# Performance work log

Measured on AMD Instinct MI355X. Metric: run time of the kernel, lower is better.

The kernel has to match this reference:

```python
import jax, jax.numpy as jnp
import numpy as np

T, B, D_IN, H = 512, 2048, 128, 16  # seq_len, batch, input_dim, hidden_dim == n_qubits


def _gate(z, theta):
    # Analytic result of the variational circuit:
    # RX(z_i) then RX(theta_i) on |0>, CNOT ladder, PauliZ on every wire
    # => <Z_k> = prod_{j<=k} cos(z_j + theta_j)
    return jnp.cumprod(jnp.cos(z + theta), axis=-1)


def setup_inputs() -> dict:
    key = jax.random.key(0)
    ks = jax.random.split(key, 13)
    fan_in = D_IN + H
    s = 1.0 / np.sqrt(fan_in)
    inputs = jax.random.normal(ks[0], (T, B, D_IN), dtype=jnp.float32)
    def lin(k):
        k1, k2 = jax.random.split(k)
        W = jax.random.uniform(k1, (H, fan_in), jnp.float32, -s, s)
        b = jax.random.uniform(k2, (H,), jnp.float32, -s, s)
        return W, b
    Wf, bf = lin(ks[1]); Wi, bi = lin(ks[2]); Wu, bu = lin(ks[3]); Wo, bo = lin(ks[4])
    theta_f = jax.random.uniform(ks[5], (H,), jnp.float32, 0.0, 2 * np.pi)
    theta_i = jax.random.uniform(ks[6], (H,), jnp.float32, 0.0, 2 * np.pi)
    theta_u = jax.random.uniform(ks[7], (H,), jnp.float32, 0.0, 2 * np.pi)
    theta_o = jax.random.uniform(ks[8], (H,), jnp.float32, 0.0, 2 * np.pi)
    return {"inputs": inputs,
            "Wf": Wf, "bf": bf, "Wi": Wi, "bi": bi,
            "Wu": Wu, "bu": bu, "Wo": Wo, "bo": bo,
            "theta_f": theta_f, "theta_i": theta_i,
            "theta_u": theta_u, "theta_o": theta_o}


def reference(inputs, Wf, bf, Wi, bi, Wu, bu, Wo, bo,
              theta_f, theta_i, theta_u, theta_o):
    Bsz = inputs.shape[1]
    h0 = jnp.zeros((Bsz, H), inputs.dtype)
    c0 = jnp.zeros((Bsz, H), inputs.dtype)

    def step(carry, x_t):
        hx, cx = carry
        comb = jnp.concatenate([x_t, hx], axis=1)          # (B, D_IN+H)
        f = jax.nn.sigmoid(_gate(comb @ Wf.T + bf, theta_f))
        i = jax.nn.sigmoid(_gate(comb @ Wi.T + bi, theta_i))
        g = jnp.tanh(_gate(comb @ Wu.T + bu, theta_u))
        o = jax.nn.sigmoid(_gate(comb @ Wo.T + bo, theta_o))
        cx = f * cx + i * g
        hx = o * jnp.tanh(cx)
        return (hx, cx), hx

    (hx, cx), outputs = jax.lax.scan(step, (h0, c0), inputs)
    return outputs, hx, cx
```

## Files before the change

kernel.cpp:

```cpp
#include <hip/hip_runtime.h>

#define T_STEPS 512
#define BATCH   2048
#define DIN     128
#define NH      16
#define COMB    (DIN + NH)

__device__ __forceinline__ float rcpf(float x)  { return __builtin_amdgcn_rcpf(x); }
__device__ __forceinline__ float sigmf(float x) { return rcpf(1.f + __expf(-x)); }
__device__ __forceinline__ float tanhf_(float x){ float e = __expf(2.f * x); return (e - 1.f) * rcpf(e + 1.f); }

template <int D>
__device__ __forceinline__ float scan_shr(float v) {
    int r = __builtin_amdgcn_update_dpp(0x3f800000, __float_as_int(v),
                                        0x110 | D, 0xF, 0xF, false);
    return __int_as_float(r);
}

__global__ __launch_bounds__(64, 2) void qlstm_kernel(
    const float* __restrict__ x,
    const float* __restrict__ Wf, const float* __restrict__ bf,
    const float* __restrict__ Wi, const float* __restrict__ bi,
    const float* __restrict__ Wu, const float* __restrict__ bu,
    const float* __restrict__ Wo, const float* __restrict__ bo,
    const float* __restrict__ thf, const float* __restrict__ thi,
    const float* __restrict__ thu, const float* __restrict__ tho,
    float* __restrict__ out)
{
    const int lane = threadIdx.x;
    const int k    = lane & 15;
    const int q    = lane >> 4;
    const int b    = blockIdx.x;

    const float* Wg[4] = {Wf, Wi, Wu, Wo};
    const float* bg[4] = {bf, bi, bu, bo};
    const float* tg[4] = {thf, thi, thu, tho};

    float w[4][32], wh[4][4], bt[4];
#pragma unroll
    for (int g = 0; g < 4; ++g) {
        const float* Wr = Wg[g] + k * COMB;
#pragma unroll
        for (int j = 0; j < 32; ++j) w[g][j] = Wr[q * 32 + j];
#pragma unroll
        for (int kk = 0; kk < 4; ++kk) wh[g][kk] = Wr[DIN + q * 4 + kk];
        bt[g] = bg[g][k] + tg[g][k];
    }

    float h = 0.f, c = 0.f;
    float cvA[32], cvB[32];

    auto xrow = [&](int t) -> const float* {
        return x + ((size_t)t * BATCH + b) * DIN + q * 32;
    };
    auto loadx = [&](float (&cv)[32], const float* p) {
#pragma unroll
        for (int j4 = 0; j4 < 8; ++j4) {
            const float4 v = *(const float4*)(p + j4 * 4);
            cv[j4 * 4 + 0] = v.x; cv[j4 * 4 + 1] = v.y;
            cv[j4 * 4 + 2] = v.z; cv[j4 * 4 + 3] = v.w;
        }
    };

    float* op = out + (size_t)b * NH + k;

    auto step = [&](int t, float (&cv)[32]) {
        float acc[4] = {0.f, 0.f, 0.f, 0.f};
#pragma unroll
        for (int j = 0; j < 32; ++j) {
#pragma unroll
            for (int g = 0; g < 4; ++g) acc[g] += cv[j] * w[g][j];
        }
#pragma unroll
        for (int kk = 0; kk < 4; ++kk) {
            const float hv = __shfl(h, q * 4 + kk, 64);
#pragma unroll
            for (int g = 0; g < 4; ++g) acc[g] += hv * wh[g][kk];
        }
#pragma unroll
        for (int g = 0; g < 4; ++g) {
            acc[g] += __shfl_xor(acc[g], 16, 64);
            acc[g] += __shfl_xor(acc[g], 32, 64);
            acc[g] = __cosf(acc[g] + bt[g]);
        }
#pragma unroll
        for (int g = 0; g < 4; ++g) {
            acc[g] *= scan_shr<1>(acc[g]);
            acc[g] *= scan_shr<2>(acc[g]);
            acc[g] *= scan_shr<4>(acc[g]);
            acc[g] *= scan_shr<8>(acc[g]);
        }
        const float f  = sigmf(acc[0]);
        const float i_ = sigmf(acc[1]);
        const float u  = tanhf_(acc[2]);
        const float o  = sigmf(acc[3]);
        c = f * c + i_ * u;
        h = o * tanhf_(c);
        if (q == 0) *op = h;
        op += (size_t)BATCH * NH;
    };

    loadx(cvA, xrow(0));
    for (int t = 0; t < T_STEPS; t += 2) {
        loadx(cvB, xrow(t + 1));
        step(t, cvA);
        const int tn = (t + 2 < T_STEPS) ? t + 2 : T_STEPS - 1;
        loadx(cvA, xrow(tn));
        step(t + 1, cvB);
    }

    if (q == 0) {
        const size_t base = (size_t)T_STEPS * BATCH * NH;
        out[base + (size_t)b * NH + k] = h;
        out[base + (size_t)BATCH * NH + (size_t)b * NH + k] = c;
    }
}

extern "C" void kernel_launch(void* const* d_in, const int* in_sizes, int n_in,
                              void* d_out, int out_size, void* d_ws, size_t ws_size,
                              hipStream_t stream) {
    const float* x   = (const float*)d_in[0];
    const float* Wf  = (const float*)d_in[1];
    const float* bf  = (const float*)d_in[2];
    const float* Wi  = (const float*)d_in[3];
    const float* bi  = (const float*)d_in[4];
    const float* Wu  = (const float*)d_in[5];
    const float* bu  = (const float*)d_in[6];
    const float* Wo  = (const float*)d_in[7];
    const float* bo  = (const float*)d_in[8];
    const float* thf = (const float*)d_in[9];
    const float* thi = (const float*)d_in[10];
    const float* thu = (const float*)d_in[11];
    const float* tho = (const float*)d_in[12];

    qlstm_kernel<<<dim3(BATCH), dim3(64), 0, stream>>>(
        x, Wf, bf, Wi, bi, Wu, bu, Wo, bo, thf, thi, thu, tho, (float*)d_out);
}
```

Measured before the change: 1.166 ms.

## Split input projection into a parallel pre-pass and lean recurrent kernel

Adds a zx_kernel that computes the input-to-gate projections (x·W plus bias and theta) for a chunk of timesteps in parallel and writes them to workspace. The recurrent kernel then handles only the 16-wide hidden matmul per step, with one lane per gate×unit, readlane broadcasts of h, a unified sigmoid/tanh activation, and bpermute gathers. This takes the large input matmul off the serial critical path. In exchange it writes and re-reads an extra 256 MB intermediate through HBM and depends on workspace size, falling back to the old kernel when no workspace is available.

```diff
diff --git a/kernel.cpp b/kernel.cpp
--- a/kernel.cpp
+++ b/kernel.cpp
@@ -5,6 +5,7 @@
 #define DIN     128
 #define NH      16
 #define COMB    (DIN + NH)
+#define G64     64
 
 __device__ __forceinline__ float rcpf(float x)  { return __builtin_amdgcn_rcpf(x); }
 __device__ __forceinline__ float sigmf(float x) { return rcpf(1.f + __expf(-x)); }
@@ -15,6 +16,142 @@
     int r = __builtin_amdgcn_update_dpp(0x3f800000, __float_as_int(v),
                                         0x110 | D, 0xF, 0xF, false);
     return __int_as_float(r);
+}
+
+__global__ __launch_bounds__(256, 4) void zx_kernel(
+    const float* __restrict__ x,
+    const float* __restrict__ Wf, const float* __restrict__ bf,
+    const float* __restrict__ Wi, const float* __restrict__ bi,
+    const float* __restrict__ Wu, const float* __restrict__ bu,
+    const float* __restrict__ Wo, const float* __restrict__ bo,
+    const float* __restrict__ thf, const float* __restrict__ thi,
+    const float* __restrict__ thu, const float* __restrict__ tho,
+    float* __restrict__ zx, int t0, int tc)
+{
+    const int tid  = threadIdx.x;
+    const int lane = tid & 63;
+    const int k    = lane & 15;
+    const int jc   = (lane >> 4) & 3;
+    const int wid  = tid >> 6;
+    const int gp   = wid & 1;
+    const int team = wid >> 1;
+
+    const float* Wg[4] = {Wf, Wi, Wu, Wo};
+    const float* bg[4] = {bf, bi, bu, bo};
+    const float* tg[4] = {thf, thi, thu, tho};
+
+    float w0[32], w1[32];
+    const float* W0 = Wg[gp * 2 + 0] + k * COMB + jc * 32;
+    const float* W1 = Wg[gp * 2 + 1] + k * COMB + jc * 32;
+#pragma unroll
+    for (int j = 0; j < 32; ++j) { w0[j] = W0[j]; w1[j] = W1[j]; }
+    const float bt0 = bg[gp * 2 + 0][k] + tg[gp * 2 + 0][k];
+    const float bt1 = bg[gp * 2 + 1][k] + tg[gp * 2 + 1][k];
+
+    const long rows  = (long)tc * BATCH;
+    const long teams = (long)gridDim.x * 2;
+    for (long r = (long)blockIdx.x * 2 + team; r < rows; r += teams) {
+        const int tl = (int)(r >> 11);
+        const int b  = (int)(r & (BATCH - 1));
+        const float* xp = x + ((size_t)(t0 + tl) * BATCH + b) * DIN + jc * 32;
+        float cv[32];
+#pragma unroll
+        for (int j4 = 0; j4 < 8; ++j4) {
+            const float4 v = *(const float4*)(xp + j4 * 4);
+            cv[j4 * 4 + 0] = v.x; cv[j4 * 4 + 1] = v.y;
+            cv[j4 * 4 + 2] = v.z; cv[j4 * 4 + 3] = v.w;
+        }
+        float a0 = 0.f, a1 = 0.f;
+#pragma unroll
+        for (int j = 0; j < 32; ++j) { a0 += cv[j] * w0[j]; a1 += cv[j] * w1[j]; }
+        a0 += __shfl_xor(a0, 16, 64); a0 += __shfl_xor(a0, 32, 64);
+        a1 += __shfl_xor(a1, 16, 64); a1 += __shfl_xor(a1, 32, 64);
+        if (jc == 0) {
+            float* zp = zx + (size_t)r * G64 + gp * 32 + k;
+            zp[0]  = a0 + bt0;
+            zp[16] = a1 + bt1;
+        }
+    }
+}
+
+__global__ __launch_bounds__(64, 2) void rec_kernel(
+    const float* __restrict__ zx,
+    const float* __restrict__ Wf, const float* __restrict__ Wi,
+    const float* __restrict__ Wu, const float* __restrict__ Wo,
+    float* __restrict__ out, int t0, int tc)
+{
+    const int lane = threadIdx.x;
+    const int k = lane & 15;
+    const int g = lane >> 4;
+    const int b = blockIdx.x;
+
+    const float* Wg[4] = {Wf, Wi, Wu, Wo};
+    float wh[16];
+    {
+        const float* Wr = Wg[g] + k * COMB + DIN;
+#pragma unroll
+        for (int kk = 0; kk < 16; ++kk) wh[kk] = Wr[kk];
+    }
+    const float sc  = (g == 2) ? 2.f : 1.f;
+    const float off = (g == 2) ? -1.f : 0.f;
+    const int i_f = k * 4, i_i = (16 + k) * 4, i_u = (32 + k) * 4, i_o = (48 + k) * 4;
+
+    const size_t sbase = (size_t)T_STEPS * BATCH * NH;
+    float h, c;
+    if (t0 == 0) { h = 0.f; c = 0.f; }
+    else {
+        h = out[sbase + (size_t)b * NH + k];
+        c = out[sbase + (size_t)BATCH * NH + (size_t)b * NH + k];
+    }
+
+    const size_t zstr = (size_t)BATCH * G64;
+    const float* zrow = zx + (size_t)b * G64 + lane;
+    auto zload = [&](int t) -> float {
+        const int tt = (t < tc) ? t : tc - 1;
+        return zrow[(size_t)tt * zstr];
+    };
+
+    float* op = out + ((size_t)t0 * BATCH + b) * NH + k;
+
+    auto step = [&](float z) {
+        float a0 = z, a1 = 0.f;
+#pragma unroll
+        for (int kk = 0; kk < 8; ++kk) {
+            const float h0 = __int_as_float(__builtin_amdgcn_readlane(__float_as_int(h), kk));
+            const float h1 = __int_as_float(__builtin_amdgcn_readlane(__float_as_int(h), kk + 8));
+            a0 += h0 * wh[kk];
+            a1 += h1 * wh[kk + 8];
+        }
+        float v = __cosf(a0 + a1);
+        v *= scan_shr<1>(v); v *= scan_shr<2>(v); v *= scan_shr<4>(v); v *= scan_shr<8>(v);
+        const float e   = __expf(-(v * sc));
+        const float s   = rcpf(1.f + e);
+        const float act = s * sc + off;
+        const int ai = __float_as_int(act);
+        const float f  = __int_as_float(__builtin_amdgcn_ds_bpermute(i_f, ai));
+        const float i_ = __int_as_float(__builtin_amdgcn_ds_bpermute(i_i, ai));
+        const float u  = __int_as_float(__builtin_amdgcn_ds_bpermute(i_u, ai));
+        const float o  = __int_as_float(__builtin_amdgcn_ds_bpermute(i_o, ai));
+        c = f * c + i_ * u;
+        const float e2 = __expf(-2.f * c);
+        const float th = (1.f - e2) * rcpf(1.f + e2);
+        h = o * th;
+        if (g == 0) *op = h;
+        op += (size_t)BATCH * NH;
+    };
+
+    float za = zload(0), zb = zload(1), zc = zload(2), zd = zload(3);
+    for (int tl = 0; tl < tc; tl += 4) {
+        step(za); za = zload(tl + 4);
+        step(zb); zb = zload(tl + 5);
+        step(zc); zc = zload(tl + 6);
+        step(zd); zd = zload(tl + 7);
+    }
+
+    if (g == 0) {
+        out[sbase + (size_t)b * NH + k] = h;
+        out[sbase + (size_t)BATCH * NH + (size_t)b * NH + k] = c;
+    }
 }
 
 __global__ __launch_bounds__(64, 2) void qlstm_kernel(
@@ -132,7 +269,28 @@
     const float* thi = (const float*)d_in[10];
     const float* thu = (const float*)d_in[11];
     const float* tho = (const float*)d_in[12];
-
-    qlstm_kernel<<<dim3(BATCH), dim3(64), 0, stream>>>(
-        x, Wf, bf, Wi, bi, Wu, bu, Wo, bo, thf, thi, thu, tho, (float*)d_out);
-}
+    float* out = (float*)d_out;
+
+    int Tc = 0;
+    const int cand[7] = {512, 256, 128, 64, 32, 16, 8};
+    for (int i = 0; i < 7; ++i) {
+        if (d_ws && (size_t)cand[i] * BATCH * G64 * sizeof(float) <= ws_size) {
+            Tc = cand[i];
+            break;
+        }
+    }
+    if (Tc == 0) {
+        qlstm_kernel<<<dim3(BATCH), dim3(64), 0, stream>>>(
+            x, Wf, bf, Wi, bi, Wu, bu, Wo, bo, thf, thi, thu, tho, out);
+        return;
+    }
+
+    float* zx = (float*)d_ws;
+    for (int t0 = 0; t0 < T_STEPS; t0 += Tc) {
+        const int tc = (T_STEPS - t0 < Tc) ? (T_STEPS - t0) : Tc;
+        zx_kernel<<<dim3(2048), dim3(256), 0, stream>>>(
+            x, Wf, bf, Wi, bi, Wu, bu, Wo, bo, thf, thi, thu, tho, zx, t0, tc);
+        rec_kernel<<<dim3(BATCH), dim3(64), 0, stream>>>(
+            zx, Wf, Wi, Wu, Wo, out, t0, tc);
+    }
+}
```

Measured after the change: 1.620 ms. +38.9%, slower.
